# Kernel optimization log

Measured on AMD Instinct MI355X. Metric: run time of the kernel, lower is better.

Reference implementation:

```python
import jax, jax.numpy as jnp
import numpy as np

PATCH = 3      # forward default patch_size
ALPHA = 1.0    # forward default alpha
# scale_factor = 1 -> F.interpolate is the identity


def setup_inputs() -> dict:
    key = jax.random.key(0)
    x_l = jax.random.normal(key, (16, 1, 1536, 1536), dtype=jnp.float32)
    return {"x_l": x_l}


def reference(x_l):
    # x_l: [N, 1, H, W]
    N, C, H, W = x_l.shape
    p = PATCH
    pad = p // 2
    # zero-padded input, matching F.unfold's implicit zero padding
    xp = jnp.pad(x_l, ((0, 0), (0, 0), (pad, pad), (pad, pad)))
    # gather the p*p shifted views -> [N, p*p, H, W] (equivalent to F.unfold for C=1;
    # softmax + weighted sum over dim 1 is permutation-invariant over the patch axis)
    local = jnp.stack(
        [xp[:, 0, i:i + H, j:j + W] for i in range(p) for j in range(p)],
        axis=1,
    )
    # local_difference = local_l - x_l**2  (broadcast over the patch dim)
    diff = local - x_l[:, 0][:, None, :, :] ** 2
    corr = jax.nn.softmax(-diff / ALPHA, axis=1)
    # softmax-weighted local average -> [N, 1, H, W]
    return jnp.sum(corr * local, axis=1, keepdims=True)
```

## Files before the change

kernel.cpp:

```cpp
#include <hip/hip_runtime.h>
#include <math.h>

#define IMG_W 1536
#define IMG_H 1536
#define NIMG  16

__global__ __launch_bounds__(128)
void WeightedAverage_55551107006568_kernel(const float* __restrict__ x,
                                           float* __restrict__ out) {
    const int wg = blockIdx.x * 128 + threadIdx.x;
    const int w0 = wg << 2;
    const int h  = blockIdx.y;
    const int n  = blockIdx.z;
    const size_t plane = (size_t)n * ((size_t)IMG_H * IMG_W);

    float v[3][6];
#pragma unroll
    for (int dr = 0; dr < 3; ++dr) {
        const int r = h + dr - 1;
        const bool rok = (r >= 0) && (r < IMG_H);
        const int rc = rok ? r : 0;
        const float* rp = x + plane + (size_t)rc * IMG_W;
        float4 m = make_float4(0.f, 0.f, 0.f, 0.f);
        if (rok) m = *(const float4*)(rp + w0);
        float lft = 0.f, rgt = 0.f;
        if (rok && w0 > 0)           lft = rp[w0 - 1];
        if (rok && (w0 + 4) < IMG_W) rgt = rp[w0 + 4];
        v[dr][0] = lft;
        v[dr][1] = m.x; v[dr][2] = m.y; v[dr][3] = m.z; v[dr][4] = m.w;
        v[dr][5] = rgt;
    }

    float colE[6], colVE[6];
#pragma unroll
    for (int c = 0; c < 6; ++c) {
        const float e0 = __expf(-v[0][c]);
        const float e1 = __expf(-v[1][c]);
        const float e2 = __expf(-v[2][c]);
        colE[c]  = e0 + e1 + e2;
        colVE[c] = v[0][c] * e0 + v[1][c] * e1 + v[2][c] * e2;
    }

    float4 o;
    float* op = &o.x;
#pragma unroll
    for (int p = 0; p < 4; ++p) {
        const float den = colE[p] + colE[p + 1] + colE[p + 2];
        const float num = colVE[p] + colVE[p + 1] + colVE[p + 2];
        op[p] = num / den;
    }
    *(float4*)(out + plane + (size_t)h * IMG_W + w0) = o;
}

extern "C" void kernel_launch(void* const* d_in, const int* in_sizes, int n_in,
                              void* d_out, int out_size, void* d_ws, size_t ws_size,
                              hipStream_t stream) {
    const float* x = (const float*)d_in[0];
    float* out = (float*)d_out;
    dim3 grid(IMG_W / (128 * 4), IMG_H, NIMG);
    dim3 block(128, 1, 1);
    WeightedAverage_55551107006568_kernel<<<grid, block, 0, stream>>>(x, out);
}
```

Baseline: 267.5 us.

## Stream 8 rows per block with rolling horizontal sums and lane shuffles for halos

Each thread now handles a vertical strip of 8 output rows. It keeps a rolling 3-row buffer of horizontally summed exp and value*exp terms, so each input row is loaded and exponentiated once instead of three times. Left and right halo values come from neighbouring lanes via shuffles, and only wave-edge lanes do scalar loads. It also switches to a fast divide and nontemporal stores, at the cost of fewer blocks and a longer serial loop per thread.

```diff
diff --git a/kernel.cpp b/kernel.cpp
--- a/kernel.cpp
+++ b/kernel.cpp
@@ -4,52 +4,66 @@
 #define IMG_W 1536
 #define IMG_H 1536
 #define NIMG  16
+#define ROWS_PER_BLOCK 8
+
+typedef float f32x4 __attribute__((ext_vector_type(4)));
 
 __global__ __launch_bounds__(128)
 void WeightedAverage_55551107006568_kernel(const float* __restrict__ x,
                                            float* __restrict__ out) {
-    const int wg = blockIdx.x * 128 + threadIdx.x;
-    const int w0 = wg << 2;
-    const int h  = blockIdx.y;
-    const int n  = blockIdx.z;
-    const size_t plane = (size_t)n * ((size_t)IMG_H * IMG_W);
+    const int lane = threadIdx.x & 63;
+    const int g  = blockIdx.x * 128 + threadIdx.x;
+    const int w0 = g << 2;
+    const int h0 = blockIdx.y * ROWS_PER_BLOCK;
+    const size_t plane = (size_t)blockIdx.z * ((size_t)IMG_H * IMG_W);
+    const float* xp = x + plane;
+    float* op = out + plane;
 
-    float v[3][6];
+    float hE[3][4], hVE[3][4];
+
 #pragma unroll
-    for (int dr = 0; dr < 3; ++dr) {
-        const int r = h + dr - 1;
-        const bool rok = (r >= 0) && (r < IMG_H);
-        const int rc = rok ? r : 0;
-        const float* rp = x + plane + (size_t)rc * IMG_W;
-        float4 m = make_float4(0.f, 0.f, 0.f, 0.f);
-        if (rok) m = *(const float4*)(rp + w0);
-        float lft = 0.f, rgt = 0.f;
-        if (rok && w0 > 0)           lft = rp[w0 - 1];
-        if (rok && (w0 + 4) < IMG_W) rgt = rp[w0 + 4];
-        v[dr][0] = lft;
-        v[dr][1] = m.x; v[dr][2] = m.y; v[dr][3] = m.z; v[dr][4] = m.w;
-        v[dr][5] = rgt;
+    for (int i = 0; i < ROWS_PER_BLOCK + 2; ++i) {
+        const int r = h0 - 1 + i;
+        const int s = i % 3;
+
+        if (r < 0 || r >= IMG_H) {
+#pragma unroll
+            for (int p = 0; p < 4; ++p) { hE[s][p] = 3.f; hVE[s][p] = 0.f; }
+        } else {
+            const float* rp = xp + (size_t)r * IMG_W + w0;
+            const f32x4 m = *(const f32x4*)rp;
+            const float e0 = __expf(-m.x), e1 = __expf(-m.y);
+            const float e2 = __expf(-m.z), e3 = __expf(-m.w);
+            const float v0 = m.x * e0, v1 = m.y * e1;
+            const float v2 = m.z * e2, v3 = m.w * e3;
+            float eL = __shfl_up(e3, 1),   vL = __shfl_up(v3, 1);
+            float eR = __shfl_down(e0, 1), vR = __shfl_down(v0, 1);
+            if (lane == 0) {
+                if (w0 == 0) { eL = 1.f; vL = 0.f; }
+                else { const float t = rp[-1]; eL = __expf(-t); vL = t * eL; }
+            }
+            if (lane == 63) {
+                if (w0 + 4 >= IMG_W) { eR = 1.f; vR = 0.f; }
+                else { const float t = rp[4]; eR = __expf(-t); vR = t * eR; }
+            }
+            hE[s][0] = eL + e0 + e1;  hVE[s][0] = vL + v0 + v1;
+            hE[s][1] = e0 + e1 + e2;  hVE[s][1] = v0 + v1 + v2;
+            hE[s][2] = e1 + e2 + e3;  hVE[s][2] = v1 + v2 + v3;
+            hE[s][3] = e2 + e3 + eR;  hVE[s][3] = v2 + v3 + vR;
+        }
+
+        if (i >= 2) {
+            const int ro = r - 1;
+            f32x4 o;
+#pragma unroll
+            for (int p = 0; p < 4; ++p) {
+                const float den = hE[0][p] + hE[1][p] + hE[2][p];
+                const float num = hVE[0][p] + hVE[1][p] + hVE[2][p];
+                o[p] = __fdividef(num, den);
+            }
+            __builtin_nontemporal_store(o, (f32x4*)(op + (size_t)ro * IMG_W + w0));
+        }
     }
-
-    float colE[6], colVE[6];
-#pragma unroll
-    for (int c = 0; c < 6; ++c) {
-        const float e0 = __expf(-v[0][c]);
-        const float e1 = __expf(-v[1][c]);
-        const float e2 = __expf(-v[2][c]);
-        colE[c]  = e0 + e1 + e2;
-        colVE[c] = v[0][c] * e0 + v[1][c] * e1 + v[2][c] * e2;
-    }
-
-    float4 o;
-    float* op = &o.x;
-#pragma unroll
-    for (int p = 0; p < 4; ++p) {
-        const float den = colE[p] + colE[p + 1] + colE[p + 2];
-        const float num = colVE[p] + colVE[p + 1] + colVE[p + 2];
-        op[p] = num / den;
-    }
-    *(float4*)(out + plane + (size_t)h * IMG_W + w0) = o;
 }
 
 extern "C" void kernel_launch(void* const* d_in, const int* in_sizes, int n_in,
@@ -57,7 +71,7 @@
                               hipStream_t stream) {
     const float* x = (const float*)d_in[0];
     float* out = (float*)d_out;
-    dim3 grid(IMG_W / (128 * 4), IMG_H, NIMG);
+    dim3 grid(IMG_W / (128 * 4), IMG_H / ROWS_PER_BLOCK, NIMG);
     dim3 block(128, 1, 1);
     WeightedAverage_55551107006568_kernel<<<grid, block, 0, stream>>>(x, out);
 }
```

New measurement: 272.5 us. About the same (+1.9%).
